# Optimization experiments

Measured on AMD Instinct MI355X. Metric: run time of the kernel, lower is better.

## Reference

```python
import jax, jax.numpy as jnp
import numpy as np

BINS = 64
PH, PW = 32, 32
WIN = 5

def setup_inputs() -> dict:
    key = jax.random.key(0)
    sinogram = jax.random.uniform(key, (64, 1, 384, 384), dtype=jnp.float32)
    return {"sinogram": sinogram}

def _extract_patches(x, n_rows, n_cols):
    # x: (B, H, W) -> non-overlapping (B, n_rows*n_cols, PH*PW), matching F.unfold
    B = x.shape[0]
    x = x.reshape(B, n_rows, PH, n_cols, PW)
    x = x.transpose(0, 1, 3, 2, 4)  # (B, n_rows, n_cols, PH, PW)
    return x.reshape(B, n_rows * n_cols, PH * PW)

def reference(sinogram):
    B, C, H, W = sinogram.shape
    # minmax window-normalize per (B, C)
    eps = 1e-6
    s_min = sinogram.min(axis=(2, 3), keepdims=True)
    s_max = sinogram.max(axis=(2, 3), keepdims=True)
    sino_norm = jnp.clip((sinogram - s_min) / (s_max - s_min + eps), 0.0, 1.0)
    # bin values into [0, BINS-1]
    sino_binned = jnp.clip((sino_norm * (BINS - 1)).astype(jnp.int32), 0, BINS - 1)

    n_rows, n_cols = H // PH, W // PW
    P = PH * PW
    patches_all = _extract_patches(sino_binned[:, 0], n_rows, n_cols)  # (B, NP, P) int32
    patches_all_f = patches_all.astype(jnp.float32)

    # selected patches: every other grid position
    grid = patches_all.reshape(B, n_rows, n_cols, P)
    patches_sel = grid[:, ::2, ::2, :].reshape(B, -1, P)  # (B, 36, P)
    n_sel = patches_sel.shape[1]

    # candidate neighborhood indices per selected patch
    indices_1d = jnp.arange(n_rows * n_cols).reshape(n_rows, n_cols)
    selected_idx = indices_1d[::2, ::2].reshape(-1)  # (36,)
    t_row = selected_idx // n_cols
    t_col = selected_idx % n_cols
    r = WIN // 2
    d = jnp.arange(-r, r + 1)
    rr = jnp.clip(t_row[:, None, None] + d[None, :, None], 0, n_rows - 1)
    cc = jnp.clip(t_col[:, None, None] + d[None, None, :], 0, n_cols - 1)
    cand_idx = (rr * n_cols + cc).reshape(-1, WIN * WIN)  # (36, 25)

    # brute-force L1 nearest-neighbor search over local candidates
    cand_patches = patches_all_f[:, cand_idx, :]  # (B, 36, 25, P)
    p_target = patches_sel.astype(jnp.float32)[:, :, None, :]
    dist = jnp.abs(p_target - cand_patches).sum(axis=-1)  # (B, 36, 25)
    self_mask = (cand_idx == selected_idx[:, None]).astype(jnp.float32)
    dist = dist + self_mask[None] * 1e9
    best_local = jnp.argmin(dist, axis=2)  # (B, 36)
    best_idx = jnp.take_along_axis(
        jnp.broadcast_to(cand_idx[None], (B,) + cand_idx.shape),
        best_local[:, :, None], axis=2)[..., 0]  # (B, 36)
    best_patches = jnp.take_along_axis(patches_all, best_idx[:, :, None], axis=1)  # (B, 36, P) int32

    # joint histogram MI
    BN = B * n_sel
    joint_idx = (patches_sel * BINS + best_patches).reshape(BN, P)
    joint_hist = jnp.zeros((BN, BINS * BINS), jnp.float32)
    joint_hist = joint_hist.at[jnp.arange(BN)[:, None], joint_idx].add(1.0)
    joint_prob = joint_hist / P
    jp2 = joint_prob.reshape(BN, BINS, BINS)
    p_x = jp2.sum(axis=2)
    p_y = jp2.sum(axis=1)
    heps = 1e-8
    h_x = -jnp.sum(p_x * jnp.log(p_x + heps), axis=1)
    h_y = -jnp.sum(p_y * jnp.log(p_y + heps), axis=1)
    h_xy = -jnp.sum(joint_prob * jnp.log(joint_prob + heps), axis=1)
    mi = (h_x + h_y - h_xy).reshape(B, n_sel)
    mi = jnp.where(jnp.isnan(mi), 0.0, mi)
    return jnp.log1p(mi)
```

## Files before the change

### kernel.cpp

```cpp
#include <hip/hip_runtime.h>
#include <math.h>

#define NB   64
#define H_   384
#define W_   384
#define NR   12
#define NC   12
#define NP   144
#define PE   1024
#define NSEL 36
#define NPART 8


__global__ __launch_bounds__(256) void k_minmax(const float* __restrict__ sino,
                                                float* __restrict__ pmin,
                                                float* __restrict__ pmax){
    int b = blockIdx.x >> 3;
    int part = blockIdx.x & 7;
    const float4* src = (const float4*)(sino + (size_t)b * (H_ * W_));
    int base = part * 4608 + threadIdx.x;
    float mn = 1e30f, mx = -1e30f;
    #pragma unroll
    for (int k = 0; k < 18; k++){
        float4 v = src[base + k * 256];
        mn = fminf(mn, fminf(fminf(v.x, v.y), fminf(v.z, v.w)));
        mx = fmaxf(mx, fmaxf(fmaxf(v.x, v.y), fmaxf(v.z, v.w)));
    }
    #pragma unroll
    for (int off = 32; off > 0; off >>= 1){
        mn = fminf(mn, __shfl_down(mn, off));
        mx = fmaxf(mx, __shfl_down(mx, off));
    }
    __shared__ float smn[4], smx[4];
    int lane = threadIdx.x & 63, wv = threadIdx.x >> 6;
    if (lane == 0){ smn[wv] = mn; smx[wv] = mx; }
    __syncthreads();
    if (threadIdx.x == 0){
        mn = fminf(fminf(smn[0], smn[1]), fminf(smn[2], smn[3]));
        mx = fmaxf(fmaxf(smx[0], smx[1]), fmaxf(smx[2], smx[3]));
        pmin[b * NPART + part] = mn;
        pmax[b * NPART + part] = mx;
    }
}

__device__ inline int binval(float x, float mn, float denom){
    float nrm = (x - mn) / denom;
    nrm = fminf(fmaxf(nrm, 0.0f), 1.0f);
    int bn = (int)(nrm * 63.0f);
    bn = bn < 0 ? 0 : (bn > 63 ? 63 : bn);
    return bn;
}

__global__ __launch_bounds__(256) void k_bin(const float* __restrict__ sino,
                                             const float* __restrict__ pmin,
                                             const float* __restrict__ pmax,
                                             unsigned char* __restrict__ pat){
    int b = blockIdx.x / NP;
    int p = blockIdx.x % NP;
    int pr = p / NC, pc = p % NC;
    float mn = 1e30f, mx = -1e30f;
    #pragma unroll
    for (int k = 0; k < NPART; k++){
        mn = fminf(mn, pmin[b * NPART + k]);
        mx = fmaxf(mx, pmax[b * NPART + k]);
    }
    float denom = mx - mn + 1e-6f;
    int tid = threadIdx.x;
    int i  = tid >> 3;
    int j4 = (tid & 7) << 2;
    const float* rowp = sino + ((size_t)b * H_ + (size_t)(pr * 32 + i)) * W_ + pc * 32 + j4;
    float4 v = *(const float4*)rowp;
    uchar4 o;
    o.x = (unsigned char)binval(v.x, mn, denom);
    o.y = (unsigned char)binval(v.y, mn, denom);
    o.z = (unsigned char)binval(v.z, mn, denom);
    o.w = (unsigned char)binval(v.w, mn, denom);
    *(uchar4*)(pat + (size_t)blockIdx.x * PE + tid * 4) = o;
}

__device__ inline unsigned int bytesad(unsigned int a, unsigned int b, unsigned int acc){
#if __has_builtin(__builtin_amdgcn_sad_u8)
    return __builtin_amdgcn_sad_u8(a, b, acc);
#else
    unsigned int s = acc;
    #pragma unroll
    for (int k = 0; k < 4; k++){
        int av = (a >> (8 * k)) & 255;
        int bv = (b >> (8 * k)) & 255;
        int d = av - bv;
        s += (unsigned int)(d < 0 ? -d : d);
    }
    return s;
#endif
}

__global__ __launch_bounds__(256) void k_mi(const unsigned char* __restrict__ pat,
                                            float* __restrict__ out){
    int b = blockIdx.x / NSEL;
    int s = blockIdx.x % NSEL;
    int sr = (s / 6) * 2, sc = (s % 6) * 2;
    int pself = sr * NC + sc;
    const unsigned char* batch = pat + (size_t)b * NP * PE;

    __shared__ uint4 selw4[64];
    __shared__ unsigned int hist[4096];
    __shared__ unsigned int distArr[25];
    __shared__ int bestCid;
    __shared__ float sH[8];

    int tid = threadIdx.x;
    int lane = tid & 63, wv = tid >> 6;

    #pragma unroll
    for (int k = 0; k < 16; k++) hist[k * 256 + tid] = 0;
    ((unsigned int*)selw4)[tid] = ((const unsigned int*)(batch + (size_t)pself * PE))[tid];
    __syncthreads();

    for (int c = wv; c < 25; c += 4){
        int dr = c / 5 - 2, dc = c % 5 - 2;
        int rr = min(max(sr + dr, 0), NR - 1);
        int cc = min(max(sc + dc, 0), NC - 1);
        int cid = rr * NC + cc;
        unsigned int dist = 0xFFFFFFFFu;
        if (cid != pself){
            uint4 cv = ((const uint4*)(batch + (size_t)cid * PE))[lane];
            uint4 sv = selw4[lane];
            dist = bytesad(cv.x, sv.x, 0u);
            dist = bytesad(cv.y, sv.y, dist);
            dist = bytesad(cv.z, sv.z, dist);
            dist = bytesad(cv.w, sv.w, dist);
            #pragma unroll
            for (int off = 32; off > 0; off >>= 1) dist += __shfl_down(dist, off);
        }
        if (lane == 0) distArr[c] = dist;
    }
    __syncthreads();

    if (tid == 0){
        unsigned int bd = 0xFFFFFFFFu; int bc = 0;
        #pragma unroll
        for (int c = 0; c < 25; c++){
            if (distArr[c] < bd){ bd = distArr[c]; bc = c; }
        }
        int dr = bc / 5 - 2, dc = bc % 5 - 2;
        int rr = min(max(sr + dr, 0), NR - 1);
        int cc = min(max(sc + dc, 0), NC - 1);
        bestCid = rr * NC + cc;
    }
    __syncthreads();

    {
        unsigned int bw = ((const unsigned int*)(batch + (size_t)bestCid * PE))[tid];
        unsigned int sw = ((const unsigned int*)selw4)[tid];
        #pragma unroll
        for (int k = 0; k < 4; k++){
            unsigned int sv = (sw >> (8 * k)) & 255u;
            unsigned int bv = (bw >> (8 * k)) & 255u;
            atomicAdd(&hist[sv * 64 + bv], 1u);
        }
    }
    __syncthreads();

    const float invP = 1.0f / 1024.0f;
    float part = 0.0f;
    #pragma unroll
    for (int k = 0; k < 16; k++){
        unsigned int cnt = hist[k * 256 + tid];
        if (cnt){
            float pj = (float)cnt * invP;
            part -= pj * __logf(pj + 1e-8f);
        }
    }
    #pragma unroll
    for (int off = 32; off > 0; off >>= 1) part += __shfl_down(part, off);
    if (lane == 0) sH[4 + wv] = part;

    if (tid < 128){
        int isY = tid >> 6;
        int t = tid & 63;
        unsigned int cnt = 0;
        if (!isY){
            for (int k = 0; k < 64; k++) cnt += hist[t * 64 + ((k + t) & 63)];
        } else {
            for (int k = 0; k < 64; k++) cnt += hist[((k + t) & 63) * 64 + t];
        }
        float pm = (float)cnt * invP;
        float term = (cnt ? -pm * __logf(pm + 1e-8f) : 0.0f);
        #pragma unroll
        for (int off = 32; off > 0; off >>= 1) term += __shfl_down(term, off);
        if (t == 0) sH[isY] = term;
    }
    __syncthreads();

    if (tid == 0){
        float hx = sH[0], hy = sH[1];
        float hxy = sH[4] + sH[5] + sH[6] + sH[7];
        float mi = hx + hy - hxy;
        out[blockIdx.x] = log1pf(mi);
    }
}

extern "C" void kernel_launch(void* const* d_in, const int* in_sizes, int n_in,
                              void* d_out, int out_size, void* d_ws, size_t ws_size,
                              hipStream_t stream) {
    const float* sino = (const float*)d_in[0];
    float* out = (float*)d_out;
    unsigned char* ws = (unsigned char*)d_ws;
    float* pmin = (float*)ws;
    float* pmax = (float*)(ws + 2048);
    unsigned char* pat = ws + 4096;

    k_minmax<<<NB * NPART, 256, 0, stream>>>(sino, pmin, pmax);
    k_bin<<<NB * NP, 256, 0, stream>>>(sino, pmin, pmax, pat);
    k_mi<<<NB * NSEL, 256, 0, stream>>>(pat, out);
}
```

Baseline: 38.47 us.

## Coarsen bin kernel to row strips and parallelize k_mi search and marginals

The binning kernel now has each block handle a 32-row strip spanning four patches. Each thread loads four float4 values along a 512-byte row span, which gives wider coalesced reads and cuts the block count by four. In k_mi, all 25 candidate L1 distances are computed in one pass using 16-lane groups instead of looping waves over candidates, and the histogram is zeroed with uint4 stores. The X and Y marginal entropies are spread across all 256 threads with shuffle reductions instead of 128 threads each doing a 64-step serial loop. The trade-off is more per-thread work in k_bin and an extra phase of LDS reads for the marginals.

```diff
diff --git a/kernel.cpp b/kernel.cpp
--- a/kernel.cpp
+++ b/kernel.cpp
@@ -55,9 +55,11 @@
                                              const float* __restrict__ pmin,
                                              const float* __restrict__ pmax,
                                              unsigned char* __restrict__ pat){
-    int b = blockIdx.x / NP;
-    int p = blockIdx.x % NP;
-    int pr = p / NC, pc = p % NC;
+    int bid = blockIdx.x;
+    int b = bid / 36;
+    int rem = bid % 36;
+    int prow = rem / 3;
+    int strip = rem % 3;
     float mn = 1e30f, mx = -1e30f;
     #pragma unroll
     for (int k = 0; k < NPART; k++){
@@ -66,16 +68,20 @@
     }
     float denom = mx - mn + 1e-6f;
     int tid = threadIdx.x;
-    int i  = tid >> 3;
-    int j4 = (tid & 7) << 2;
-    const float* rowp = sino + ((size_t)b * H_ + (size_t)(pr * 32 + i)) * W_ + pc * 32 + j4;
-    float4 v = *(const float4*)rowp;
-    uchar4 o;
-    o.x = (unsigned char)binval(v.x, mn, denom);
-    o.y = (unsigned char)binval(v.y, mn, denom);
-    o.z = (unsigned char)binval(v.z, mn, denom);
-    o.w = (unsigned char)binval(v.w, mn, denom);
-    *(uchar4*)(pat + (size_t)blockIdx.x * PE + tid * 4) = o;
+    int irow = tid >> 3;
+    int tc   = tid & 7;
+    const float4* rowp = (const float4*)(sino + ((size_t)b * H_ + (size_t)(prow * 32 + irow)) * W_ + strip * 128);
+    unsigned char* pbase = pat + ((size_t)(b * NP + prow * NC + strip * 4)) * PE + irow * 32 + tc * 4;
+    #pragma unroll
+    for (int k = 0; k < 4; k++){
+        float4 v = rowp[tc + k * 8];
+        uchar4 o;
+        o.x = (unsigned char)binval(v.x, mn, denom);
+        o.y = (unsigned char)binval(v.y, mn, denom);
+        o.z = (unsigned char)binval(v.z, mn, denom);
+        o.w = (unsigned char)binval(v.w, mn, denom);
+        *(uchar4*)(pbase + (size_t)k * PE) = o;
+    }
 }
 
 __device__ inline unsigned int bytesad(unsigned int a, unsigned int b, unsigned int acc){
@@ -106,33 +112,45 @@
     __shared__ unsigned int hist[4096];
     __shared__ unsigned int distArr[25];
     __shared__ int bestCid;
-    __shared__ float sH[8];
+    __shared__ float sHx[4], sHy[4], sHxy[4];
 
     int tid = threadIdx.x;
     int lane = tid & 63, wv = tid >> 6;
 
-    #pragma unroll
-    for (int k = 0; k < 16; k++) hist[k * 256 + tid] = 0;
+    {
+        uint4 z = {0u, 0u, 0u, 0u};
+        uint4* h4 = (uint4*)hist;
+        #pragma unroll
+        for (int k = 0; k < 4; k++) h4[k * 256 + tid] = z;
+    }
     ((unsigned int*)selw4)[tid] = ((const unsigned int*)(batch + (size_t)pself * PE))[tid];
     __syncthreads();
 
-    for (int c = wv; c < 25; c += 4){
-        int dr = c / 5 - 2, dc = c % 5 - 2;
-        int rr = min(max(sr + dr, 0), NR - 1);
-        int cc = min(max(sc + dc, 0), NC - 1);
-        int cid = rr * NC + cc;
-        unsigned int dist = 0xFFFFFFFFu;
-        if (cid != pself){
-            uint4 cv = ((const uint4*)(batch + (size_t)cid * PE))[lane];
-            uint4 sv = selw4[lane];
-            dist = bytesad(cv.x, sv.x, 0u);
-            dist = bytesad(cv.y, sv.y, dist);
-            dist = bytesad(cv.z, sv.z, dist);
-            dist = bytesad(cv.w, sv.w, dist);
+    int grp = lane >> 4;
+    int sl  = lane & 15;
+    #pragma unroll
+    for (int r = 0; r < 2; r++){
+        int c = r * 16 + wv * 4 + grp;
+        if (c < 25){
+            int dr = c / 5 - 2, dc = c % 5 - 2;
+            int rr = min(max(sr + dr, 0), NR - 1);
+            int cc = min(max(sc + dc, 0), NC - 1);
+            int cid = rr * NC + cc;
+            const uint4* cp = (const uint4*)(batch + (size_t)cid * PE);
+            unsigned int dist = 0;
             #pragma unroll
-            for (int off = 32; off > 0; off >>= 1) dist += __shfl_down(dist, off);
-        }
-        if (lane == 0) distArr[c] = dist;
+            for (int k = 0; k < 4; k++){
+                uint4 cv = cp[sl + 16 * k];
+                uint4 sv = selw4[sl + 16 * k];
+                dist = bytesad(cv.x, sv.x, dist);
+                dist = bytesad(cv.y, sv.y, dist);
+                dist = bytesad(cv.z, sv.z, dist);
+                dist = bytesad(cv.w, sv.w, dist);
+            }
+            #pragma unroll
+            for (int off = 8; off > 0; off >>= 1) dist += __shfl_xor(dist, off);
+            if (sl == 0) distArr[c] = (cid == pself) ? 0xFFFFFFFFu : dist;
+        }
     }
     __syncthreads();
 
@@ -162,39 +180,61 @@
     __syncthreads();
 
     const float invP = 1.0f / 1024.0f;
-    float part = 0.0f;
-    #pragma unroll
-    for (int k = 0; k < 16; k++){
-        unsigned int cnt = hist[k * 256 + tid];
-        if (cnt){
-            float pj = (float)cnt * invP;
-            part -= pj * __logf(pj + 1e-8f);
-        }
-    }
-    #pragma unroll
-    for (int off = 32; off > 0; off >>= 1) part += __shfl_down(part, off);
-    if (lane == 0) sH[4 + wv] = part;
-
-    if (tid < 128){
-        int isY = tid >> 6;
-        int t = tid & 63;
+
+    {
+        float part = 0.0f;
+        #pragma unroll
+        for (int k = 0; k < 16; k++){
+            unsigned int cnt = hist[k * 256 + tid];
+            if (cnt){
+                float pj = (float)cnt * invP;
+                part -= pj * __logf(pj + 1e-8f);
+            }
+        }
+        #pragma unroll
+        for (int off = 32; off > 0; off >>= 1) part += __shfl_down(part, off);
+        if (lane == 0) sHxy[wv] = part;
+    }
+
+    {
+        int r = tid >> 2, q = tid & 3;
         unsigned int cnt = 0;
-        if (!isY){
-            for (int k = 0; k < 64; k++) cnt += hist[t * 64 + ((k + t) & 63)];
-        } else {
-            for (int k = 0; k < 64; k++) cnt += hist[((k + t) & 63) * 64 + t];
-        }
-        float pm = (float)cnt * invP;
-        float term = (cnt ? -pm * __logf(pm + 1e-8f) : 0.0f);
+        #pragma unroll
+        for (int i = 0; i < 16; i++) cnt += hist[r * 64 + q * 16 + i];
+        cnt += __shfl_xor(cnt, 1);
+        cnt += __shfl_xor(cnt, 2);
+        float term = 0.0f;
+        if (q == 0 && cnt){
+            float pm = (float)cnt * invP;
+            term = -pm * __logf(pm + 1e-8f);
+        }
         #pragma unroll
         for (int off = 32; off > 0; off >>= 1) term += __shfl_down(term, off);
-        if (t == 0) sH[isY] = term;
+        if (lane == 0) sHx[wv] = term;
+    }
+
+    {
+        int c = tid >> 2, q = tid & 3;
+        unsigned int cnt = 0;
+        #pragma unroll
+        for (int i = 0; i < 16; i++) cnt += hist[(q * 16 + i) * 64 + c];
+        cnt += __shfl_xor(cnt, 1);
+        cnt += __shfl_xor(cnt, 2);
+        float term = 0.0f;
+        if (q == 0 && cnt){
+            float pm = (float)cnt * invP;
+            term = -pm * __logf(pm + 1e-8f);
+        }
+        #pragma unroll
+        for (int off = 32; off > 0; off >>= 1) term += __shfl_down(term, off);
+        if (lane == 0) sHy[wv] = term;
     }
     __syncthreads();
 
     if (tid == 0){
-        float hx = sH[0], hy = sH[1];
-        float hxy = sH[4] + sH[5] + sH[6] + sH[7];
+        float hx  = sHx[0] + sHx[1] + sHx[2] + sHx[3];
+        float hy  = sHy[0] + sHy[1] + sHy[2] + sHy[3];
+        float hxy = sHxy[0] + sHxy[1] + sHxy[2] + sHxy[3];
         float mi = hx + hy - hxy;
         out[blockIdx.x] = log1pf(mi);
     }
@@ -211,6 +251,6 @@
     unsigned char* pat = ws + 4096;
 
     k_minmax<<<NB * NPART, 256, 0, stream>>>(sino, pmin, pmax);
-    k_bin<<<NB * NP, 256, 0, stream>>>(sino, pmin, pmax, pat);
+    k_bin<<<NB * 36, 256, 0, stream>>>(sino, pmin, pmax, pat);
     k_mi<<<NB * NSEL, 256, 0, stream>>>(pat, out);
 }
```

Result: faster. 35.74 us (-7.1%).

## Fuse binning into MI kernel with LDS-resident patch neighborhoods

Applied to the files above, without the earlier changes.

Removes the separate binning kernel and its global byte-patch buffer. Each block now bins a 5x8 patch region of the sinogram straight into LDS and runs the L1 neighbor search, joint histogram and entropy for three selected patches. The joint histogram is packed as two 16-bit counters per word, with a padded stride to reduce LDS use and bank conflicts, and the argmin becomes a wave-level min over packed keys. In exchange, overlapping regions mean the float sinogram is re-read several times, fewer and larger blocks are launched, and each block processes its three patches serially.

```diff
diff --git a/kernel.cpp b/kernel.cpp
--- a/kernel.cpp
+++ b/kernel.cpp
@@ -6,8 +6,6 @@
 #define W_   384
 #define NR   12
 #define NC   12
-#define NP   144
-#define PE   1024
 #define NSEL 36
 #define NPART 8
 
@@ -51,33 +49,6 @@
     return bn;
 }
 
-__global__ __launch_bounds__(256) void k_bin(const float* __restrict__ sino,
-                                             const float* __restrict__ pmin,
-                                             const float* __restrict__ pmax,
-                                             unsigned char* __restrict__ pat){
-    int b = blockIdx.x / NP;
-    int p = blockIdx.x % NP;
-    int pr = p / NC, pc = p % NC;
-    float mn = 1e30f, mx = -1e30f;
-    #pragma unroll
-    for (int k = 0; k < NPART; k++){
-        mn = fminf(mn, pmin[b * NPART + k]);
-        mx = fmaxf(mx, pmax[b * NPART + k]);
-    }
-    float denom = mx - mn + 1e-6f;
-    int tid = threadIdx.x;
-    int i  = tid >> 3;
-    int j4 = (tid & 7) << 2;
-    const float* rowp = sino + ((size_t)b * H_ + (size_t)(pr * 32 + i)) * W_ + pc * 32 + j4;
-    float4 v = *(const float4*)rowp;
-    uchar4 o;
-    o.x = (unsigned char)binval(v.x, mn, denom);
-    o.y = (unsigned char)binval(v.y, mn, denom);
-    o.z = (unsigned char)binval(v.z, mn, denom);
-    o.w = (unsigned char)binval(v.w, mn, denom);
-    *(uchar4*)(pat + (size_t)blockIdx.x * PE + tid * 4) = o;
-}
-
 __device__ inline unsigned int bytesad(unsigned int a, unsigned int b, unsigned int acc){
 #if __has_builtin(__builtin_amdgcn_sad_u8)
     return __builtin_amdgcn_sad_u8(a, b, acc);
@@ -94,109 +65,169 @@
 #endif
 }
 
-__global__ __launch_bounds__(256) void k_mi(const unsigned char* __restrict__ pat,
-                                            float* __restrict__ out){
-    int b = blockIdx.x / NSEL;
-    int s = blockIdx.x % NSEL;
-    int sr = (s / 6) * 2, sc = (s % 6) * 2;
-    int pself = sr * NC + sc;
-    const unsigned char* batch = pat + (size_t)b * NP * PE;
-
-    __shared__ uint4 selw4[64];
-    __shared__ unsigned int hist[4096];
+__global__ __launch_bounds__(512, 6) void k_binmi(const float* __restrict__ sino,
+                                                  const float* __restrict__ pmin,
+                                                  const float* __restrict__ pmax,
+                                                  float* __restrict__ out){
+    int bid = blockIdx.x;
+    int b = bid / 12;
+    int rem = bid - b * 12;
+    int sr6 = rem >> 1, chalf = rem & 1;
+    int sr = sr6 << 1;
+    int r0 = sr - 2; if (r0 < 0) r0 = 0;
+    int r1 = sr + 2; if (r1 > NR - 1) r1 = NR - 1;
+    int nrp = r1 - r0 + 1;
+    int c0 = chalf << 2;
+
+    __shared__ unsigned char patl[5 * 8 * 1024];
+    __shared__ unsigned int hist[2112];
     __shared__ unsigned int distArr[25];
-    __shared__ int bestCid;
-    __shared__ float sH[8];
+    __shared__ int bestOffSh;
+    __shared__ float rterm[64], cterm[64], wred[8];
 
     int tid = threadIdx.x;
     int lane = tid & 63, wv = tid >> 6;
 
-    #pragma unroll
-    for (int k = 0; k < 16; k++) hist[k * 256 + tid] = 0;
-    ((unsigned int*)selw4)[tid] = ((const unsigned int*)(batch + (size_t)pself * PE))[tid];
+    float mn = 1e30f, mx = -1e30f;
+    #pragma unroll
+    for (int k = 0; k < NPART; k++){
+        mn = fminf(mn, pmin[b * NPART + k]);
+        mx = fmaxf(mx, pmax[b * NPART + k]);
+    }
+    float denom = mx - mn + 1e-6f;
+
+    {
+        const float* sbase = sino + ((size_t)b * H_ + (size_t)r0 * 32) * W_ + c0 * 32;
+        int total4 = nrp << 11;
+        for (int idx4 = tid; idx4 < total4; idx4 += 512){
+            int r  = idx4 >> 6;
+            int cc = (idx4 & 63) << 2;
+            float4 v = *(const float4*)(sbase + (size_t)r * W_ + cc);
+            uchar4 o;
+            o.x = (unsigned char)binval(v.x, mn, denom);
+            o.y = (unsigned char)binval(v.y, mn, denom);
+            o.z = (unsigned char)binval(v.z, mn, denom);
+            o.w = (unsigned char)binval(v.w, mn, denom);
+            int pr = r >> 5, i = r & 31;
+            int pc = cc >> 5, j = cc & 31;
+            *(uchar4*)(patl + (((pr << 3) + pc) << 10) + i * 32 + j) = o;
+        }
+    }
     __syncthreads();
 
-    for (int c = wv; c < 25; c += 4){
-        int dr = c / 5 - 2, dc = c % 5 - 2;
-        int rr = min(max(sr + dr, 0), NR - 1);
-        int cc = min(max(sc + dc, 0), NC - 1);
-        int cid = rr * NC + cc;
-        unsigned int dist = 0xFFFFFFFFu;
-        if (cid != pself){
-            uint4 cv = ((const uint4*)(batch + (size_t)cid * PE))[lane];
-            uint4 sv = selw4[lane];
-            dist = bytesad(cv.x, sv.x, 0u);
-            dist = bytesad(cv.y, sv.y, dist);
-            dist = bytesad(cv.z, sv.z, dist);
-            dist = bytesad(cv.w, sv.w, dist);
-            #pragma unroll
-            for (int off = 32; off > 0; off >>= 1) dist += __shfl_down(dist, off);
-        }
-        if (lane == 0) distArr[c] = dist;
-    }
-    __syncthreads();
-
-    if (tid == 0){
-        unsigned int bd = 0xFFFFFFFFu; int bc = 0;
-        #pragma unroll
-        for (int c = 0; c < 25; c++){
-            if (distArr[c] < bd){ bd = distArr[c]; bc = c; }
-        }
-        int dr = bc / 5 - 2, dc = bc % 5 - 2;
-        int rr = min(max(sr + dr, 0), NR - 1);
-        int cc = min(max(sc + dc, 0), NC - 1);
-        bestCid = rr * NC + cc;
-    }
-    __syncthreads();
-
-    {
-        unsigned int bw = ((const unsigned int*)(batch + (size_t)bestCid * PE))[tid];
-        unsigned int sw = ((const unsigned int*)selw4)[tid];
-        #pragma unroll
-        for (int k = 0; k < 4; k++){
-            unsigned int sv = (sw >> (8 * k)) & 255u;
-            unsigned int bv = (bw >> (8 * k)) & 255u;
-            atomicAdd(&hist[sv * 64 + bv], 1u);
-        }
-    }
-    __syncthreads();
-
     const float invP = 1.0f / 1024.0f;
-    float part = 0.0f;
-    #pragma unroll
-    for (int k = 0; k < 16; k++){
-        unsigned int cnt = hist[k * 256 + tid];
-        if (cnt){
-            float pj = (float)cnt * invP;
-            part -= pj * __logf(pj + 1e-8f);
-        }
-    }
-    #pragma unroll
-    for (int off = 32; off > 0; off >>= 1) part += __shfl_down(part, off);
-    if (lane == 0) sH[4 + wv] = part;
-
-    if (tid < 128){
-        int isY = tid >> 6;
-        int t = tid & 63;
-        unsigned int cnt = 0;
-        if (!isY){
-            for (int k = 0; k < 64; k++) cnt += hist[t * 64 + ((k + t) & 63)];
-        } else {
-            for (int k = 0; k < 64; k++) cnt += hist[((k + t) & 63) * 64 + t];
-        }
-        float pm = (float)cnt * invP;
-        float term = (cnt ? -pm * __logf(pm + 1e-8f) : 0.0f);
-        #pragma unroll
-        for (int off = 32; off > 0; off >>= 1) term += __shfl_down(term, off);
-        if (t == 0) sH[isY] = term;
-    }
-    __syncthreads();
-
-    if (tid == 0){
-        float hx = sH[0], hy = sH[1];
-        float hxy = sH[4] + sH[5] + sH[6] + sH[7];
-        float mi = hx + hy - hxy;
-        out[blockIdx.x] = log1pf(mi);
+    for (int si = 0; si < 3; si++){
+        int scS = chalf * 6 + si * 2;
+        int pself = sr * NC + scS;
+        int selOff = (((sr - r0) << 3) + (scS - c0)) << 10;
+
+        for (int k = tid; k < 2112; k += 512) hist[k] = 0;
+
+        int grp = tid >> 4, sl = tid & 15;
+        if (grp < 25){
+            int dr = grp / 5 - 2, dc = grp % 5 - 2;
+            int rr = sr + dr;  rr = rr < 0 ? 0 : (rr > NR - 1 ? NR - 1 : rr);
+            int cc2 = scS + dc; cc2 = cc2 < 0 ? 0 : (cc2 > NC - 1 ? NC - 1 : cc2);
+            int cid = rr * NC + cc2;
+            const uint4* cp = (const uint4*)(patl + ((((rr - r0) << 3) + (cc2 - c0)) << 10));
+            const uint4* sp = (const uint4*)(patl + selOff);
+            unsigned int dist = 0;
+            #pragma unroll
+            for (int k = 0; k < 4; k++){
+                uint4 cv = cp[sl + (k << 4)];
+                uint4 sv = sp[sl + (k << 4)];
+                dist = bytesad(cv.x, sv.x, dist);
+                dist = bytesad(cv.y, sv.y, dist);
+                dist = bytesad(cv.z, sv.z, dist);
+                dist = bytesad(cv.w, sv.w, dist);
+            }
+            #pragma unroll
+            for (int off = 8; off > 0; off >>= 1) dist += __shfl_xor(dist, off);
+            if (sl == 0) distArr[grp] = (cid == pself) ? 0x00FFFFFFu : dist;
+        }
+        __syncthreads();
+
+        if (tid < 64){
+            unsigned int key = (tid < 25) ? (distArr[tid] * 32u + (unsigned int)tid)
+                                          : 0xFFFFFFFFu;
+            #pragma unroll
+            for (int off = 32; off > 0; off >>= 1){
+                unsigned int o = __shfl_xor(key, off);
+                if (o < key) key = o;
+            }
+            if (tid == 0){
+                int bc = (int)(key & 31u);
+                int dr = bc / 5 - 2, dc = bc % 5 - 2;
+                int rr = sr + dr;  rr = rr < 0 ? 0 : (rr > NR - 1 ? NR - 1 : rr);
+                int cc2 = scS + dc; cc2 = cc2 < 0 ? 0 : (cc2 > NC - 1 ? NC - 1 : cc2);
+                bestOffSh = (((rr - r0) << 3) + (cc2 - c0)) << 10;
+            }
+        }
+        __syncthreads();
+
+        {
+            int boff = bestOffSh;
+            unsigned int sw = *(const unsigned short*)(patl + selOff + tid * 2);
+            unsigned int bw = *(const unsigned short*)(patl + boff  + tid * 2);
+            unsigned int sv0 = sw & 255u, sv1 = (sw >> 8) & 255u;
+            unsigned int bv0 = bw & 255u, bv1 = (bw >> 8) & 255u;
+            atomicAdd(&hist[sv0 * 33 + (bv0 >> 1)], 1u << ((bv0 & 1) << 4));
+            atomicAdd(&hist[sv1 * 33 + (bv1 >> 1)], 1u << ((bv1 & 1) << 4));
+        }
+        __syncthreads();
+
+        {
+            float part = 0.0f;
+            #pragma unroll
+            for (int k = 0; k < 5; k++){
+                int w = tid + (k << 9);
+                if (w < 2112){
+                    unsigned int hv = hist[w];
+                    unsigned int clo = hv & 0xFFFFu, chi = hv >> 16;
+                    if (clo){ float p = (float)clo * invP; part -= p * __logf(p + 1e-8f); }
+                    if (chi){ float p = (float)chi * invP; part -= p * __logf(p + 1e-8f); }
+                }
+            }
+            #pragma unroll
+            for (int off = 32; off > 0; off >>= 1) part += __shfl_down(part, off);
+            if (lane == 0) wred[wv] = part;
+        }
+        {
+            int sv = tid >> 3, q = tid & 7;
+            unsigned int cnt = 0;
+            #pragma unroll
+            for (int i2 = 0; i2 < 4; i2++){
+                unsigned int hv = hist[sv * 33 + q * 4 + i2];
+                cnt += (hv & 0xFFFFu) + (hv >> 16);
+            }
+            cnt += __shfl_xor(cnt, 1); cnt += __shfl_xor(cnt, 2); cnt += __shfl_xor(cnt, 4);
+            if (q == 0){
+                float pm = (float)cnt * invP;
+                rterm[sv] = cnt ? -pm * __logf(pm + 1e-8f) : 0.0f;
+            }
+        }
+        {
+            int bv = tid >> 3, q = tid & 7;
+            int w0 = bv >> 1, sh = (bv & 1) << 4;
+            unsigned int cnt = 0;
+            #pragma unroll
+            for (int m = 0; m < 8; m++){
+                cnt += (hist[(q * 8 + m) * 33 + w0] >> sh) & 0xFFFFu;
+            }
+            cnt += __shfl_xor(cnt, 1); cnt += __shfl_xor(cnt, 2); cnt += __shfl_xor(cnt, 4);
+            if (q == 0){
+                float pm = (float)cnt * invP;
+                cterm[bv] = cnt ? -pm * __logf(pm + 1e-8f) : 0.0f;
+            }
+        }
+        __syncthreads();
+
+        if (tid < 64){
+            float val = rterm[tid] + cterm[tid] - (tid < 8 ? wred[tid] : 0.0f);
+            #pragma unroll
+            for (int off = 32; off > 0; off >>= 1) val += __shfl_down(val, off);
+            if (tid == 0) out[b * NSEL + sr6 * 6 + chalf * 3 + si] = log1pf(val);
+        }
     }
 }
 
@@ -208,9 +239,7 @@
     unsigned char* ws = (unsigned char*)d_ws;
     float* pmin = (float*)ws;
     float* pmax = (float*)(ws + 2048);
-    unsigned char* pat = ws + 4096;
 
     k_minmax<<<NB * NPART, 256, 0, stream>>>(sino, pmin, pmax);
-    k_bin<<<NB * NP, 256, 0, stream>>>(sino, pmin, pmax, pat);
-    k_mi<<<NB * NSEL, 256, 0, stream>>>(pat, out);
-}
+    k_binmi<<<NB * 12, 512, 0, stream>>>(sino, pmin, pmax, out);
+}
```

New measurement: 43.85 us. +14.0%, slower.
